# Kernel tuning notes

Measured on AMD Instinct MI355X. Metric: run time of the kernel, lower is better.

The kernel has to match this reference:

```python
import jax, jax.numpy as jnp
import numpy as np
import math

B, N, E, L = 64, 2048, 8192, 50
IN_DIM, HID, HEADS, R, BASES = 128, 64, 3, 5, 4
NODE_NUM = 100000


def setup_inputs() -> dict:
    key = jax.random.key(0)
    ks = jax.random.split(key, 16)
    node_ids = jax.random.randint(ks[0], (B, N), 0, NODE_NUM)
    edge_index = jax.random.randint(ks[1], (B, 2, E), 0, N)
    edge_type = jax.random.randint(ks[2], (B, E), 0, R)
    sent_ids = jax.random.randint(ks[3], (B, L), 0, N)
    # embedding table, padding_idx=0 row zeroed, init N(0, 1/input_dim)
    emb_table = jax.random.normal(ks[4], (NODE_NUM, IN_DIM), jnp.float32) / IN_DIM
    emb_table = emb_table.at[0].set(0.0)
    # RGCN basis decomposition params
    bases = jax.random.normal(ks[5], (BASES, IN_DIM, IN_DIM), jnp.float32) * (1.0 / math.sqrt(IN_DIM))
    comp = jax.random.normal(ks[6], (R, BASES), jnp.float32) * 0.5
    root_w = jax.random.normal(ks[7], (IN_DIM, IN_DIM), jnp.float32) * (1.0 / math.sqrt(IN_DIM))
    root_b = jnp.zeros((IN_DIM,), jnp.float32)
    # attention weights: 3 heads concatenated along output dim -> [IN_DIM, 3*HID]
    xav = math.sqrt(6.0 / (IN_DIM + HID))
    wq = jax.random.uniform(ks[8], (IN_DIM, HEADS * HID), jnp.float32, -xav, xav)
    wk = jax.random.uniform(ks[9], (IN_DIM, HEADS * HID), jnp.float32, -xav, xav)
    wv = jax.random.uniform(ks[10], (IN_DIM, HEADS * HID), jnp.float32, -xav, xav)
    attn_w = jax.random.normal(ks[11], (HEADS * HID, 1), jnp.float32) * 0.05
    attn_b = jnp.zeros((1,), jnp.float32)
    fc_w = jax.random.normal(ks[12], (HEADS * HID, 1), jnp.float32) * 0.05
    fc_b = jnp.zeros((1,), jnp.float32)
    return {"emb_table": emb_table, "bases": bases, "comp": comp, "root_w": root_w,
            "root_b": root_b, "wq": wq, "wk": wk, "wv": wv, "attn_w": attn_w,
            "attn_b": attn_b, "fc_w": fc_w, "fc_b": fc_b, "node_ids": node_ids,
            "edge_index": edge_index, "edge_type": edge_type, "sent_ids": sent_ids}


def _rgcn_conv(x, ei, et, W, root_w, root_b):
    # x: [N, D], ei: [2, E], et: [E], W: [R, D, D]
    src, tgt = ei[0], ei[1]
    msg = jnp.einsum('ei,eio->eo', x[src], W[et])            # [E, D]
    # per-(target, relation) mean normalization (PyG RGCNConv default)
    key = tgt * R + et
    deg = jax.ops.segment_sum(jnp.ones((et.shape[0],), x.dtype), key, num_segments=N * R)
    norm = 1.0 / jnp.maximum(deg[key], 1.0)
    agg = jax.ops.segment_sum(msg * norm[:, None], tgt, num_segments=N)  # [N, D]
    return agg + x @ root_w + root_b


def reference(emb_table, bases, comp, root_w, root_b, wq, wk, wv,
              attn_w, attn_b, fc_w, fc_b, node_ids, edge_index, edge_type, sent_ids):
    # relation weights from basis decomposition: [R, D, D]
    W = jnp.einsum('rb,bio->rio', comp, bases)
    x = emb_table[node_ids]                                   # [B, N, D]
    x_upd = jax.vmap(_rgcn_conv, in_axes=(0, 0, 0, None, None, None))(
        x, edge_index, edge_type, W, root_w, root_b)          # [B, N, D]
    X = jnp.take_along_axis(x_upd, sent_ids[:, :, None], axis=1)  # [B, L, D]
    # self-attention with head-concatenated Q/K/V (single softmax over 3*HID dims)
    Q = X @ wq                                                # [B, L, 3H]
    K = X @ wk
    V = X @ wv
    scores = jax.nn.softmax(jnp.einsum('bld,bmd->blm', Q, K) / math.sqrt(HEADS * HID), axis=-1)
    H = jnp.einsum('blm,bmd->bld', scores, V)                 # [B, L, 3H]
    attn = H @ attn_w + attn_b                                # [B, L, 1]
    pooled = jnp.sum(H * attn, axis=1)                        # [B, 3H]
    return jax.nn.sigmoid(pooled @ fc_w + fc_b)               # [B, 1]
```

## Files before the change

### kernel.cpp

```cpp
#include <hip/hip_runtime.h>
#include <math.h>

#define BDIM 64
#define NN   2048
#define EE   8192
#define LL   50
#define DD   128
#define RR   5
#define NBASES 4
#define H3   192
#define RECCAP 1024
#define KDIM 768
#define GROWS 16

__device__ __forceinline__ void fma4(float4& a, float s, const float4& w) {
    a.x = fmaf(s, w.x, a.x); a.y = fmaf(s, w.y, a.y);
    a.z = fmaf(s, w.z, a.z); a.w = fmaf(s, w.w, a.w);
}

__global__ __launch_bounds__(256) void precompute_all(
        const float* __restrict__ bases, const float* __restrict__ comp,
        const float* __restrict__ root_w, const float* __restrict__ wq,
        const float* __restrict__ wk, const float* __restrict__ wv,
        const float* __restrict__ attn_w, const float* __restrict__ fc_w,
        float* __restrict__ Wcat, float* __restrict__ A,
        float* __restrict__ va, float* __restrict__ vf, float* __restrict__ acc) {
    int blk = blockIdx.x, t = threadIdx.x;
    if (blk < 384) {
        int idx = blk * 256 + t;
        int k = idx >> 7, o = idx & 127;
        if (k < DD) {
            Wcat[idx] = root_w[idx];
        } else {
            int r = (k - DD) >> 7, i = (k - DD) & 127;
            float s = 0.f;
#pragma unroll
            for (int bb = 0; bb < NBASES; ++bb)
                s += comp[r * NBASES + bb] * bases[bb * DD * DD + i * DD + o];
            Wcat[idx] = s;
        }
    } else if (blk < 512) {
        int i = blk - 384;
        __shared__ float wqs[H3];
        if (t < H3) wqs[t] = wq[i * H3 + t];
        __syncthreads();
        if (t < DD) {
            const float4* wkr = (const float4*)(wk + t * H3);
            float s = 0.f;
#pragma unroll
            for (int d4 = 0; d4 < H3 / 4; ++d4) {
                float4 v = wkr[d4];
                s += wqs[4*d4]*v.x + wqs[4*d4+1]*v.y + wqs[4*d4+2]*v.z + wqs[4*d4+3]*v.w;
            }
            A[i * DD + t] = s;
        }
    } else {
        if (t < DD) {
            const float4* wr = (const float4*)(wv + t * H3);
            float a = 0.f, f = 0.f;
#pragma unroll
            for (int d4 = 0; d4 < H3 / 4; ++d4) {
                float4 v = wr[d4];
                a += v.x*attn_w[4*d4] + v.y*attn_w[4*d4+1] + v.z*attn_w[4*d4+2] + v.w*attn_w[4*d4+3];
                f += v.x*fc_w[4*d4] + v.y*fc_w[4*d4+1] + v.z*fc_w[4*d4+2] + v.w*fc_w[4*d4+3];
            }
            va[t] = a; vf[t] = f;
        } else if (t < DD + BDIM) {
            acc[t - DD] = 0.f;
        }
    }
}

__global__ __launch_bounds__(512) void matchseg(const int* __restrict__ edge_index,
                                                const int* __restrict__ edge_type,
                                                const int* __restrict__ sent_ids,
                                                int* __restrict__ rep,
                                                int* __restrict__ segoff,
                                                int* __restrict__ recbuf2) {
    int b = blockIdx.x, t = threadIdx.x;
    __shared__ int mark[NN];
    __shared__ int scnt[LL * RR];
    __shared__ int soff[LL * RR + 1];
    __shared__ int scan[256];
    __shared__ int recs[RECCAP];
    __shared__ int lcnt;

    for (int i = t; i < NN; i += 512) mark[i] = -1;
    if (t < LL * RR) scnt[t] = 0;
    if (t == 0) lcnt = 0;
    __syncthreads();
    const int* sb = sent_ids + b * LL;
    if (t < LL) mark[sb[t]] = t;
    __syncthreads();
    if (t < LL) rep[b * LL + t] = mark[sb[t]];

    const int* src_arr = edge_index + (size_t)b * 2 * EE;
    const int* tgt_arr = src_arr + EE;
    const int* et_arr  = edge_type + (size_t)b * EE;
    const int4* tgt4 = (const int4*)tgt_arr;
    for (int i4 = t; i4 < EE / 4; i4 += 512) {
        int4 v = tgt4[i4];
        int e0 = 4 * i4;
        int lv[4] = {mark[v.x], mark[v.y], mark[v.z], mark[v.w]};
#pragma unroll
        for (int k = 0; k < 4; ++k) {
            int l = lv[k];
            if (l >= 0) {
                int e = e0 + k;
                int r = et_arr[e];
                int s = src_arr[e];
                int pos = atomicAdd(&lcnt, 1);
                if (pos < RECCAP) {
                    recs[pos] = (l << 14) | (r << 11) | s;
                    atomicAdd(&scnt[l * RR + r], 1);
                }
            }
        }
    }
    __syncthreads();
    if (t < 256) scan[t] = (t < LL * RR) ? scnt[t] : 0;
    __syncthreads();
    for (int off = 1; off < 256; off <<= 1) {
        int v = 0;
        if (t < 256 && t >= off) v = scan[t - off];
        __syncthreads();
        if (t < 256) scan[t] += v;
        __syncthreads();
    }
    if (t == 0) soff[0] = 0;
    if (t < LL * RR) soff[t + 1] = scan[t];
    if (t < LL * RR) scnt[t] = 0;
    __syncthreads();
    if (t <= LL * RR) segoff[b * (LL * RR + 1) + t] = soff[t];
    int nm = (lcnt < RECCAP) ? lcnt : RECCAP;
    for (int i = t; i < nm; i += 512) {
        int rc = recs[i];
        int key = (rc >> 14) * RR + ((rc >> 11) & 7);
        int pos = soff[key] + atomicAdd(&scnt[key], 1);
        recbuf2[b * RECCAP + pos] = rc;
    }
}

__global__ __launch_bounds__(64) void aggregate(const float* __restrict__ emb,
                                                const int* __restrict__ node_ids,
                                                const int* __restrict__ sent_ids,
                                                const int* __restrict__ rep,
                                                const int* __restrict__ segoff,
                                                const int* __restrict__ recbuf2,
                                                float* __restrict__ U) {
    int bl = blockIdx.x;
    int b  = bl / LL;
    int lane = threadIdx.x;
    const int* nid = node_ids + (size_t)b * NN;
    int myrep = rep[bl];
    const int* so = segoff + b * (LL * RR + 1) + myrep * RR;
    const int* rb = recbuf2 + b * RECCAP;
    float* Urow = U + (size_t)bl * KDIM;

    int row = nid[sent_ids[bl]];
    Urow[lane]      = emb[(size_t)row * DD + lane];
    Urow[lane + 64] = emb[(size_t)row * DD + 64 + lane];

#pragma unroll
    for (int r = 0; r < RR; ++r) {
        int s0 = so[r], s1 = so[r + 1];
        float a0 = 0.f, a1 = 0.f;
        for (int j = s0; j < s1; ++j) {
            int s = rb[j] & 2047;
            int rw = nid[s];
            a0 += emb[(size_t)rw * DD + lane];
            a1 += emb[(size_t)rw * DD + 64 + lane];
        }
        float inv = (s1 > s0) ? 1.f / (float)(s1 - s0) : 0.f;
        Urow[DD + r * DD + lane]      = a0 * inv;
        Urow[DD + r * DD + 64 + lane] = a1 * inv;
    }
}

__global__ __launch_bounds__(256) void gemm_fused(const float* __restrict__ U,
                                                  const float* __restrict__ Wcat,
                                                  const float* __restrict__ A,
                                                  const float* __restrict__ root_b,
                                                  const float* __restrict__ va,
                                                  const float* __restrict__ vf,
                                                  float* __restrict__ Xws,
                                                  float* __restrict__ XAws,
                                                  float* __restrict__ pv,
                                                  float* __restrict__ qv) {
    __shared__ float Us[GROWS][KDIM];
    __shared__ float Xs[GROWS][DD];
    __shared__ float vas[DD], vfs[DD];

    int t = threadIdx.x;
    int row0 = blockIdx.x * GROWS;
    int tx = t & 31, ty = t >> 5;
    int m0 = 2 * ty, m1 = m0 + 1;
    int c0 = 4 * tx;

    const float4* Ug = (const float4*)(U + (size_t)row0 * KDIM);
    for (int i = t; i < GROWS * KDIM / 4; i += 256) ((float4*)Us)[i] = Ug[i];
    if (t < DD) { vas[t] = va[t]; vfs[t] = vf[t]; }
    __syncthreads();

    float4 rb = *(const float4*)(root_b + c0);
    float4 acc0 = rb, acc1 = rb;
    const float4* Wc4 = (const float4*)Wcat;
    const float4* u0p = (const float4*)Us[m0];
    const float4* u1p = (const float4*)Us[m1];
#pragma unroll 2
    for (int k4 = 0; k4 < KDIM / 4; ++k4) {
        float4 u0 = u0p[k4], u1 = u1p[k4];
        int k = 4 * k4;
        float4 w0 = Wc4[(k + 0) * 32 + tx];
        float4 w1 = Wc4[(k + 1) * 32 + tx];
        float4 w2 = Wc4[(k + 2) * 32 + tx];
        float4 w3 = Wc4[(k + 3) * 32 + tx];
        fma4(acc0, u0.x, w0); fma4(acc1, u1.x, w0);
        fma4(acc0, u0.y, w1); fma4(acc1, u1.y, w1);
        fma4(acc0, u0.z, w2); fma4(acc1, u1.z, w2);
        fma4(acc0, u0.w, w3); fma4(acc1, u1.w, w3);
    }
    *(float4*)&Xs[m0][c0] = acc0;
    *(float4*)&Xs[m1][c0] = acc1;
    *(float4*)(Xws + (size_t)(row0 + m0) * DD + c0) = acc0;
    *(float4*)(Xws + (size_t)(row0 + m1) * DD + c0) = acc1;
    __syncthreads();

    float4 z0 = {0,0,0,0}, z1 = {0,0,0,0};
    const float4* A4 = (const float4*)A;
    const float4* x0p = (const float4*)Xs[m0];
    const float4* x1p = (const float4*)Xs[m1];
#pragma unroll 2
    for (int k4 = 0; k4 < DD / 4; ++k4) {
        float4 x0 = x0p[k4], x1 = x1p[k4];
        int k = 4 * k4;
        float4 a0 = A4[(k + 0) * 32 + tx];
        float4 a1 = A4[(k + 1) * 32 + tx];
        float4 a2 = A4[(k + 2) * 32 + tx];
        float4 a3 = A4[(k + 3) * 32 + tx];
        fma4(z0, x0.x, a0); fma4(z1, x1.x, a0);
        fma4(z0, x0.y, a1); fma4(z1, x1.y, a1);
        fma4(z0, x0.z, a2); fma4(z1, x1.z, a2);
        fma4(z0, x0.w, a3); fma4(z1, x1.w, a3);
    }
    *(float4*)(XAws + (size_t)(row0 + m0) * DD + c0) = z0;
    *(float4*)(XAws + (size_t)(row0 + m1) * DD + c0) = z1;

    int lane = t & 63, w = t >> 6;
#pragma unroll
    for (int rr = 0; rr < 4; ++rr) {
        int m = 4 * w + rr;
        float xv0 = Xs[m][lane], xv1 = Xs[m][lane + 64];
        float pp = xv0 * vas[lane] + xv1 * vas[lane + 64];
        float qq = xv0 * vfs[lane] + xv1 * vfs[lane + 64];
#pragma unroll
        for (int off = 32; off; off >>= 1) {
            pp += __shfl_xor(pp, off);
            qq += __shfl_xor(qq, off);
        }
        if (lane == 0) { pv[row0 + m] = pp; qv[row0 + m] = qq; }
    }
}

__global__ __launch_bounds__(64) void attn_row(const float* __restrict__ Xws,
                                               const float* __restrict__ XAws,
                                               const float* __restrict__ pv,
                                               const float* __restrict__ qv,
                                               const float* __restrict__ attn_b,
                                               float* __restrict__ acc) {
    int bl = blockIdx.x;
    int b  = bl / LL;
    int lane = threadIdx.x;
    const float* Xb = Xws + (size_t)b * LL * DD;
    const float* xa = XAws + (size_t)bl * DD;
    float xa0 = xa[lane], xa1 = xa[lane + 64];

    float myS = 0.f;
    for (int m = 0; m < LL; m += 2) {
        const float* xm0 = Xb + m * DD;
        const float* xm1 = xm0 + DD;
        float p0 = xa0 * xm0[lane] + xa1 * xm0[lane + 64];
        float p1 = xa0 * xm1[lane] + xa1 * xm1[lane + 64];
#pragma unroll
        for (int off = 32; off; off >>= 1) {
            p0 += __shfl_xor(p0, off);
            p1 += __shfl_xor(p1, off);
        }
        if (lane == m)     myS = p0;
        if (lane == m + 1) myS = p1;
    }
    const float scale = 0.07216878364870322f;
    float sval = (lane < LL) ? myS * scale : -INFINITY;
    float mx = sval;
#pragma unroll
    for (int off = 32; off; off >>= 1) mx = fmaxf(mx, __shfl_xor(mx, off));
    float e = (lane < LL) ? __expf(sval - mx) : 0.f;
    float sum = e;
#pragma unroll
    for (int off = 32; off; off >>= 1) sum += __shfl_xor(sum, off);
    float inv = 1.f / sum;
    float sm = e * inv;
    float pa = (lane < LL) ? sm * pv[b * LL + lane] : 0.f;
    float qa = (lane < LL) ? sm * qv[b * LL + lane] : 0.f;
#pragma unroll
    for (int off = 32; off; off >>= 1) {
        pa += __shfl_xor(pa, off);
        qa += __shfl_xor(qa, off);
    }
    if (lane == 0) atomicAdd(&acc[b], (pa + attn_b[0]) * qa);
}

__global__ __launch_bounds__(64) void finalize(const float* __restrict__ acc,
                                               const float* __restrict__ fc_b,
                                               float* __restrict__ out) {
    int b = threadIdx.x;
    if (b < BDIM) out[b] = 1.f / (1.f + expf(-(acc[b] + fc_b[0])));
}

extern "C" void kernel_launch(void* const* d_in, const int* in_sizes, int n_in,
                              void* d_out, int out_size, void* d_ws, size_t ws_size,
                              hipStream_t stream) {
    const float* emb     = (const float*)d_in[0];
    const float* bases   = (const float*)d_in[1];
    const float* comp    = (const float*)d_in[2];
    const float* root_w  = (const float*)d_in[3];
    const float* root_b  = (const float*)d_in[4];
    const float* wq      = (const float*)d_in[5];
    const float* wk      = (const float*)d_in[6];
    const float* wv      = (const float*)d_in[7];
    const float* attn_w  = (const float*)d_in[8];
    const float* attn_b  = (const float*)d_in[9];
    const float* fc_w    = (const float*)d_in[10];
    const float* fc_b    = (const float*)d_in[11];
    const int* node_ids  = (const int*)d_in[12];
    const int* edge_index= (const int*)d_in[13];
    const int* edge_type = (const int*)d_in[14];
    const int* sent_ids  = (const int*)d_in[15];
    float* out = (float*)d_out;

    float* ws = (float*)d_ws;
    float* Wcat = ws;
    float* A    = ws + 98304;
    float* va   = ws + 114688;
    float* vf   = ws + 114816;
    float* acc  = ws + 114944;
    float* pv   = ws + 115008;
    float* qv   = ws + 118208;
    float* Xws  = ws + 121408;
    float* XAws = ws + 531008;
    float* U    = ws + 940608;
    int* rep     = (int*)(ws + 3398208);
    int* segoff  = (int*)(ws + 3401408);
    int* recbuf2 = (int*)(ws + 3417472);

    hipLaunchKernelGGL(precompute_all, dim3(513), dim3(256), 0, stream,
                       bases, comp, root_w, wq, wk, wv, attn_w, fc_w,
                       Wcat, A, va, vf, acc);
    hipLaunchKernelGGL(matchseg, dim3(BDIM), dim3(512), 0, stream,
                       edge_index, edge_type, sent_ids, rep, segoff, recbuf2);
    hipLaunchKernelGGL(aggregate, dim3(BDIM * LL), dim3(64), 0, stream,
                       emb, node_ids, sent_ids, rep, segoff, recbuf2, U);
    hipLaunchKernelGGL(gemm_fused, dim3(BDIM * LL / GROWS), dim3(256), 0, stream,
                       U, Wcat, A, root_b, va, vf, Xws, XAws, pv, qv);
    hipLaunchKernelGGL(attn_row, dim3(BDIM * LL), dim3(64), 0, stream,
                       Xws, XAws, pv, qv, attn_b, acc);
    hipLaunchKernelGGL(finalize, dim3(1), dim3(64), 0, stream, acc, fc_b, out);
}
```

Before: 212.9 us.

## Fuse gather-aggregate into GEMM kernel and merge attention with finalize per batch

The neighbor aggregation is moved into the GEMM kernel, where each wavefront gathers one row straight into shared memory, so the U workspace round trip and a separate launch disappear. The GEMM tile shrinks to 8 rows with 512 threads, one wave per row and two outputs per lane. The per-row attention kernel, the atomic accumulation and the finalize kernel are replaced by one block per batch that stages X transposed and XA in shared memory and writes the sigmoid output directly. In exchange, the Wcat loads are reused across fewer rows per block, and the attention stage runs on only 64 blocks.

Result: slower. 251.8 us (+18.3%).

```diff
diff --git a/kernel.cpp b/kernel.cpp
--- a/kernel.cpp
+++ b/kernel.cpp
@@ -11,12 +11,7 @@
 #define H3   192
 #define RECCAP 1024
 #define KDIM 768
-#define GROWS 16
-
-__device__ __forceinline__ void fma4(float4& a, float s, const float4& w) {
-    a.x = fmaf(s, w.x, a.x); a.y = fmaf(s, w.y, a.y);
-    a.z = fmaf(s, w.z, a.z); a.w = fmaf(s, w.w, a.w);
-}
+#define GROWS 8
 
 __global__ __launch_bounds__(256) void precompute_all(
         const float* __restrict__ bases, const float* __restrict__ comp,
@@ -24,7 +19,7 @@
         const float* __restrict__ wk, const float* __restrict__ wv,
         const float* __restrict__ attn_w, const float* __restrict__ fc_w,
         float* __restrict__ Wcat, float* __restrict__ A,
-        float* __restrict__ va, float* __restrict__ vf, float* __restrict__ acc) {
+        float* __restrict__ va, float* __restrict__ vf) {
     int blk = blockIdx.x, t = threadIdx.x;
     if (blk < 384) {
         int idx = blk * 256 + t;
@@ -65,8 +60,6 @@
                 f += v.x*fc_w[4*d4] + v.y*fc_w[4*d4+1] + v.z*fc_w[4*d4+2] + v.w*fc_w[4*d4+3];
             }
             va[t] = a; vf[t] = f;
-        } else if (t < DD + BDIM) {
-            acc[t - DD] = 0.f;
         }
     }
 }
@@ -141,48 +134,17 @@
     }
 }
 
-__global__ __launch_bounds__(64) void aggregate(const float* __restrict__ emb,
-                                                const int* __restrict__ node_ids,
-                                                const int* __restrict__ sent_ids,
-                                                const int* __restrict__ rep,
-                                                const int* __restrict__ segoff,
-                                                const int* __restrict__ recbuf2,
-                                                float* __restrict__ U) {
-    int bl = blockIdx.x;
-    int b  = bl / LL;
-    int lane = threadIdx.x;
-    const int* nid = node_ids + (size_t)b * NN;
-    int myrep = rep[bl];
-    const int* so = segoff + b * (LL * RR + 1) + myrep * RR;
-    const int* rb = recbuf2 + b * RECCAP;
-    float* Urow = U + (size_t)bl * KDIM;
-
-    int row = nid[sent_ids[bl]];
-    Urow[lane]      = emb[(size_t)row * DD + lane];
-    Urow[lane + 64] = emb[(size_t)row * DD + 64 + lane];
-
-#pragma unroll
-    for (int r = 0; r < RR; ++r) {
-        int s0 = so[r], s1 = so[r + 1];
-        float a0 = 0.f, a1 = 0.f;
-        for (int j = s0; j < s1; ++j) {
-            int s = rb[j] & 2047;
-            int rw = nid[s];
-            a0 += emb[(size_t)rw * DD + lane];
-            a1 += emb[(size_t)rw * DD + 64 + lane];
-        }
-        float inv = (s1 > s0) ? 1.f / (float)(s1 - s0) : 0.f;
-        Urow[DD + r * DD + lane]      = a0 * inv;
-        Urow[DD + r * DD + 64 + lane] = a1 * inv;
-    }
-}
-
-__global__ __launch_bounds__(256) void gemm_fused(const float* __restrict__ U,
+__global__ __launch_bounds__(512) void gemm_fused(const float* __restrict__ emb,
                                                   const float* __restrict__ Wcat,
                                                   const float* __restrict__ A,
                                                   const float* __restrict__ root_b,
                                                   const float* __restrict__ va,
                                                   const float* __restrict__ vf,
+                                                  const int* __restrict__ node_ids,
+                                                  const int* __restrict__ sent_ids,
+                                                  const int* __restrict__ rep,
+                                                  const int* __restrict__ segoff,
+                                                  const int* __restrict__ recbuf2,
                                                   float* __restrict__ Xws,
                                                   float* __restrict__ XAws,
                                                   float* __restrict__ pv,
@@ -192,129 +154,149 @@
     __shared__ float vas[DD], vfs[DD];
 
     int t = threadIdx.x;
+    int w = t >> 6, lane = t & 63;
     int row0 = blockIdx.x * GROWS;
-    int tx = t & 31, ty = t >> 5;
-    int m0 = 2 * ty, m1 = m0 + 1;
-    int c0 = 4 * tx;
-
-    const float4* Ug = (const float4*)(U + (size_t)row0 * KDIM);
-    for (int i = t; i < GROWS * KDIM / 4; i += 256) ((float4*)Us)[i] = Ug[i];
+    int bl = row0 + w;
+    int b  = bl / LL;
+    const int* nid = node_ids + (size_t)b * NN;
+
+    {
+        int myrep = rep[bl];
+        const int* so = segoff + b * (LL * RR + 1) + myrep * RR;
+        const int* rb = recbuf2 + b * RECCAP;
+        int nrow = nid[sent_ids[bl]];
+        Us[w][lane]      = emb[(size_t)nrow * DD + lane];
+        Us[w][lane + 64] = emb[(size_t)nrow * DD + 64 + lane];
+#pragma unroll
+        for (int r = 0; r < RR; ++r) {
+            int s0 = so[r], s1 = so[r + 1];
+            float a0 = 0.f, a1 = 0.f;
+            for (int j = s0; j < s1; ++j) {
+                int s = rb[j] & 2047;
+                int rw = nid[s];
+                a0 += emb[(size_t)rw * DD + lane];
+                a1 += emb[(size_t)rw * DD + 64 + lane];
+            }
+            float inv = (s1 > s0) ? 1.f / (float)(s1 - s0) : 0.f;
+            Us[w][DD + r * DD + lane]      = a0 * inv;
+            Us[w][DD + r * DD + 64 + lane] = a1 * inv;
+        }
+    }
     if (t < DD) { vas[t] = va[t]; vfs[t] = vf[t]; }
     __syncthreads();
 
-    float4 rb = *(const float4*)(root_b + c0);
-    float4 acc0 = rb, acc1 = rb;
-    const float4* Wc4 = (const float4*)Wcat;
-    const float4* u0p = (const float4*)Us[m0];
-    const float4* u1p = (const float4*)Us[m1];
+    int tc = lane;
+    float2 acc = *(const float2*)(root_b + 2 * tc);
+    const float2* W2 = (const float2*)Wcat;
+    const float4* u4 = (const float4*)Us[w];
 #pragma unroll 2
     for (int k4 = 0; k4 < KDIM / 4; ++k4) {
-        float4 u0 = u0p[k4], u1 = u1p[k4];
+        float4 u = u4[k4];
         int k = 4 * k4;
-        float4 w0 = Wc4[(k + 0) * 32 + tx];
-        float4 w1 = Wc4[(k + 1) * 32 + tx];
-        float4 w2 = Wc4[(k + 2) * 32 + tx];
-        float4 w3 = Wc4[(k + 3) * 32 + tx];
-        fma4(acc0, u0.x, w0); fma4(acc1, u1.x, w0);
-        fma4(acc0, u0.y, w1); fma4(acc1, u1.y, w1);
-        fma4(acc0, u0.z, w2); fma4(acc1, u1.z, w2);
-        fma4(acc0, u0.w, w3); fma4(acc1, u1.w, w3);
-    }
-    *(float4*)&Xs[m0][c0] = acc0;
-    *(float4*)&Xs[m1][c0] = acc1;
-    *(float4*)(Xws + (size_t)(row0 + m0) * DD + c0) = acc0;
-    *(float4*)(Xws + (size_t)(row0 + m1) * DD + c0) = acc1;
-    __syncthreads();
-
-    float4 z0 = {0,0,0,0}, z1 = {0,0,0,0};
-    const float4* A4 = (const float4*)A;
-    const float4* x0p = (const float4*)Xs[m0];
-    const float4* x1p = (const float4*)Xs[m1];
+        float2 w0 = W2[(k + 0) * 64 + tc];
+        float2 w1 = W2[(k + 1) * 64 + tc];
+        float2 w2 = W2[(k + 2) * 64 + tc];
+        float2 w3 = W2[(k + 3) * 64 + tc];
+        acc.x = fmaf(u.x, w0.x, acc.x); acc.y = fmaf(u.x, w0.y, acc.y);
+        acc.x = fmaf(u.y, w1.x, acc.x); acc.y = fmaf(u.y, w1.y, acc.y);
+        acc.x = fmaf(u.z, w2.x, acc.x); acc.y = fmaf(u.z, w2.y, acc.y);
+        acc.x = fmaf(u.w, w3.x, acc.x); acc.y = fmaf(u.w, w3.y, acc.y);
+    }
+    *(float2*)&Xs[w][2 * tc] = acc;
+    *(float2*)(Xws + (size_t)bl * DD + 2 * tc) = acc;
+
+    float2 z = {0.f, 0.f};
+    const float2* A2 = (const float2*)A;
+    const float4* x4 = (const float4*)Xs[w];
 #pragma unroll 2
     for (int k4 = 0; k4 < DD / 4; ++k4) {
-        float4 x0 = x0p[k4], x1 = x1p[k4];
+        float4 x = x4[k4];
         int k = 4 * k4;
-        float4 a0 = A4[(k + 0) * 32 + tx];
-        float4 a1 = A4[(k + 1) * 32 + tx];
-        float4 a2 = A4[(k + 2) * 32 + tx];
-        float4 a3 = A4[(k + 3) * 32 + tx];
-        fma4(z0, x0.x, a0); fma4(z1, x1.x, a0);
-        fma4(z0, x0.y, a1); fma4(z1, x1.y, a1);
-        fma4(z0, x0.z, a2); fma4(z1, x1.z, a2);
-        fma4(z0, x0.w, a3); fma4(z1, x1.w, a3);
-    }
-    *(float4*)(XAws + (size_t)(row0 + m0) * DD + c0) = z0;
-    *(float4*)(XAws + (size_t)(row0 + m1) * DD + c0) = z1;
-
-    int lane = t & 63, w = t >> 6;
-#pragma unroll
-    for (int rr = 0; rr < 4; ++rr) {
-        int m = 4 * w + rr;
-        float xv0 = Xs[m][lane], xv1 = Xs[m][lane + 64];
-        float pp = xv0 * vas[lane] + xv1 * vas[lane + 64];
-        float qq = xv0 * vfs[lane] + xv1 * vfs[lane + 64];
+        float2 a0 = A2[(k + 0) * 64 + tc];
+        float2 a1 = A2[(k + 1) * 64 + tc];
+        float2 a2 = A2[(k + 2) * 64 + tc];
+        float2 a3 = A2[(k + 3) * 64 + tc];
+        z.x = fmaf(x.x, a0.x, z.x); z.y = fmaf(x.x, a0.y, z.y);
+        z.x = fmaf(x.y, a1.x, z.x); z.y = fmaf(x.y, a1.y, z.y);
+        z.x = fmaf(x.z, a2.x, z.x); z.y = fmaf(x.z, a2.y, z.y);
+        z.x = fmaf(x.w, a3.x, z.x); z.y = fmaf(x.w, a3.y, z.y);
+    }
+    *(float2*)(XAws + (size_t)bl * DD + 2 * tc) = z;
+
+    float pp = acc.x * vas[2 * tc] + acc.y * vas[2 * tc + 1];
+    float qq = acc.x * vfs[2 * tc] + acc.y * vfs[2 * tc + 1];
+#pragma unroll
+    for (int off = 32; off; off >>= 1) {
+        pp += __shfl_xor(pp, off);
+        qq += __shfl_xor(qq, off);
+    }
+    if (lane == 0) { pv[bl] = pp; qv[bl] = qq; }
+}
+
+__global__ __launch_bounds__(256) void attn_batch(const float* __restrict__ Xws,
+                                                  const float* __restrict__ XAws,
+                                                  const float* __restrict__ pv,
+                                                  const float* __restrict__ qv,
+                                                  const float* __restrict__ attn_b,
+                                                  const float* __restrict__ fc_b,
+                                                  float* __restrict__ out) {
+    __shared__ float4 XT4[32][64];
+    __shared__ float4 XA4[LL][32];
+    __shared__ float pvs[64], qvs[64];
+    __shared__ float partial[4];
+
+    int b = blockIdx.x, t = threadIdx.x;
+    int w = t >> 6, lane = t & 63;
+
+    const float4* Xb4  = (const float4*)(Xws  + (size_t)b * LL * DD);
+    const float4* XAb4 = (const float4*)(XAws + (size_t)b * LL * DD);
+    for (int idx = t; idx < LL * 32; idx += 256) {
+        int m = idx >> 5, k = idx & 31;
+        XT4[k][m] = Xb4[idx];
+        ((float4*)XA4)[idx] = XAb4[idx];
+    }
+    if (t < 64) {
+        pvs[t] = (t < LL) ? pv[b * LL + t] : 0.f;
+        qvs[t] = (t < LL) ? qv[b * LL + t] : 0.f;
+    }
+    __syncthreads();
+
+    const float scale = 0.07216878364870322f;
+    float ab = attn_b[0];
+    float local = 0.f;
+    for (int l = w; l < LL; l += 4) {
+        float s = 0.f;
+#pragma unroll
+        for (int kk = 0; kk < 32; ++kk) {
+            float4 xa = XA4[l][kk];
+            float4 xt = XT4[kk][lane];
+            s = fmaf(xa.x, xt.x, s);
+            s = fmaf(xa.y, xt.y, s);
+            s = fmaf(xa.z, xt.z, s);
+            s = fmaf(xa.w, xt.w, s);
+        }
+        s *= scale;
+        float sval = (lane < LL) ? s : -INFINITY;
+        float mx = sval;
+#pragma unroll
+        for (int off = 32; off; off >>= 1) mx = fmaxf(mx, __shfl_xor(mx, off));
+        float e = (lane < LL) ? __expf(sval - mx) : 0.f;
+        float sum = e, pa = e * pvs[lane], qa = e * qvs[lane];
 #pragma unroll
         for (int off = 32; off; off >>= 1) {
-            pp += __shfl_xor(pp, off);
-            qq += __shfl_xor(qq, off);
-        }
-        if (lane == 0) { pv[row0 + m] = pp; qv[row0 + m] = qq; }
-    }
-}
-
-__global__ __launch_bounds__(64) void attn_row(const float* __restrict__ Xws,
-                                               const float* __restrict__ XAws,
-                                               const float* __restrict__ pv,
-                                               const float* __restrict__ qv,
-                                               const float* __restrict__ attn_b,
-                                               float* __restrict__ acc) {
-    int bl = blockIdx.x;
-    int b  = bl / LL;
-    int lane = threadIdx.x;
-    const float* Xb = Xws + (size_t)b * LL * DD;
-    const float* xa = XAws + (size_t)bl * DD;
-    float xa0 = xa[lane], xa1 = xa[lane + 64];
-
-    float myS = 0.f;
-    for (int m = 0; m < LL; m += 2) {
-        const float* xm0 = Xb + m * DD;
-        const float* xm1 = xm0 + DD;
-        float p0 = xa0 * xm0[lane] + xa1 * xm0[lane + 64];
-        float p1 = xa0 * xm1[lane] + xa1 * xm1[lane + 64];
-#pragma unroll
-        for (int off = 32; off; off >>= 1) {
-            p0 += __shfl_xor(p0, off);
-            p1 += __shfl_xor(p1, off);
-        }
-        if (lane == m)     myS = p0;
-        if (lane == m + 1) myS = p1;
-    }
-    const float scale = 0.07216878364870322f;
-    float sval = (lane < LL) ? myS * scale : -INFINITY;
-    float mx = sval;
-#pragma unroll
-    for (int off = 32; off; off >>= 1) mx = fmaxf(mx, __shfl_xor(mx, off));
-    float e = (lane < LL) ? __expf(sval - mx) : 0.f;
-    float sum = e;
-#pragma unroll
-    for (int off = 32; off; off >>= 1) sum += __shfl_xor(sum, off);
-    float inv = 1.f / sum;
-    float sm = e * inv;
-    float pa = (lane < LL) ? sm * pv[b * LL + lane] : 0.f;
-    float qa = (lane < LL) ? sm * qv[b * LL + lane] : 0.f;
-#pragma unroll
-    for (int off = 32; off; off >>= 1) {
-        pa += __shfl_xor(pa, off);
-        qa += __shfl_xor(qa, off);
-    }
-    if (lane == 0) atomicAdd(&acc[b], (pa + attn_b[0]) * qa);
-}
-
-__global__ __launch_bounds__(64) void finalize(const float* __restrict__ acc,
-                                               const float* __restrict__ fc_b,
-                                               float* __restrict__ out) {
-    int b = threadIdx.x;
-    if (b < BDIM) out[b] = 1.f / (1.f + expf(-(acc[b] + fc_b[0])));
+            sum += __shfl_xor(sum, off);
+            pa  += __shfl_xor(pa, off);
+            qa  += __shfl_xor(qa, off);
+        }
+        float inv = 1.f / sum;
+        local += (pa * inv + ab) * (qa * inv);
+    }
+    if (lane == 0) partial[w] = local;
+    __syncthreads();
+    if (t == 0) {
+        float s = partial[0] + partial[1] + partial[2] + partial[3];
+        out[b] = 1.f / (1.f + expf(-(s + fc_b[0])));
+    }
 }
 
 extern "C" void kernel_launch(void* const* d_in, const int* in_sizes, int n_in,
@@ -343,26 +325,22 @@
     float* A    = ws + 98304;
     float* va   = ws + 114688;
     float* vf   = ws + 114816;
-    float* acc  = ws + 114944;
-    float* pv   = ws + 115008;
-    float* qv   = ws + 118208;
-    float* Xws  = ws + 121408;
-    float* XAws = ws + 531008;
-    float* U    = ws + 940608;
-    int* rep     = (int*)(ws + 3398208);
-    int* segoff  = (int*)(ws + 3401408);
-    int* recbuf2 = (int*)(ws + 3417472);
+    float* pv   = ws + 114944;
+    float* qv   = ws + 118144;
+    float* Xws  = ws + 121344;
+    float* XAws = ws + 530944;
+    int* rep     = (int*)(ws + 940544);
+    int* segoff  = (int*)(ws + 943744);
+    int* recbuf2 = (int*)(ws + 959808);
 
     hipLaunchKernelGGL(precompute_all, dim3(513), dim3(256), 0, stream,
                        bases, comp, root_w, wq, wk, wv, attn_w, fc_w,
-                       Wcat, A, va, vf, acc);
+                       Wcat, A, va, vf);
     hipLaunchKernelGGL(matchseg, dim3(BDIM), dim3(512), 0, stream,
                        edge_index, edge_type, sent_ids, rep, segoff, recbuf2);
-    hipLaunchKernelGGL(aggregate, dim3(BDIM * LL), dim3(64), 0, stream,
-                       emb, node_ids, sent_ids, rep, segoff, recbuf2, U);
-    hipLaunchKernelGGL(gemm_fused, dim3(BDIM * LL / GROWS), dim3(256), 0, stream,
-                       U, Wcat, A, root_b, va, vf, Xws, XAws, pv, qv);
-    hipLaunchKernelGGL(attn_row, dim3(BDIM * LL), dim3(64), 0, stream,
-                       Xws, XAws, pv, qv, attn_b, acc);
-    hipLaunchKernelGGL(finalize, dim3(1), dim3(64), 0, stream, acc, fc_b, out);
-}
+    hipLaunchKernelGGL(gemm_fused, dim3(BDIM * LL / GROWS), dim3(512), 0, stream,
+                       emb, Wcat, A, root_b, va, vf, node_ids, sent_ids,
+                       rep, segoff, recbuf2, Xws, XAws, pv, qv);
+    hipLaunchKernelGGL(attn_batch, dim3(BDIM), dim3(256), 0, stream,
+                       Xws, XAws, pv, qv, attn_b, fc_b, out);
+}
```
